# Optimization experiments

Measured on AMD Instinct MI355X. Metric: run time of the kernel, lower is better.

## Reference

```python
import jax, jax.numpy as jnp
import numpy as np

# ---- quantization constants (8-bit, per-tensor affine; representative values) ----
Q_MAX = 255.0
S_IN, Z_IN = 0.05, 128.0      # block input
S1, Z1 = 0.04, 128.0          # after expand 1x1 + hardswish
S2, Z2 = 0.04, 128.0          # after depthwise 5x5 + hardswish
S_SE1, Z_SE1 = 0.03, 128.0    # SE fc1 output
S_SE2, Z_SE2 = 1.0 / 255.0, 0.0  # SE fc2 hardsigmoid output in [0,1]
S_MUL, Z_MUL = 0.04, 128.0    # SE gated activation
S3, Z3 = 0.05, 128.0          # after project 1x1
S_OUT, Z_OUT = 0.06, 128.0    # after residual add
W_SCALE = 0.01                # symmetric per-tensor weight scale (zero_point = 0)
EXP_C = 576                   # expanded channels (depthwise groups)


def conv(x, w, stride=1, padding=0, groups=1):
    return jax.lax.conv_general_dilated(
        x, w, (stride, stride), [(padding, padding), (padding, padding)],
        feature_group_count=groups, dimension_numbers=('NCHW', 'OIHW', 'NCHW'))


def hardswish(x):
    return x * jnp.clip(x + 3.0, 0.0, 6.0) * (1.0 / 6.0)


def hardsigmoid(x):
    return jnp.clip(x + 3.0, 0.0, 6.0) * (1.0 / 6.0)


def qconv(x_q, w_q, b_q, s_in, z_in, s_out, z_out, stride=1, padding=0, groups=1, act=None):
    """Quantized conv: int-domain accumulation (simulated in fp32), fused activation
    on the dequantized accumulator, then requantize to [0, Q_MAX]."""
    acc = conv(x_q - z_in, w_q, stride, padding, groups) + b_q[None, :, None, None]
    deq = acc * (s_in * W_SCALE)  # dequantize accumulator
    if act == 'hardswish':
        deq = hardswish(deq)
    elif act == 'hardsigmoid':
        deq = hardsigmoid(deq)
    return jnp.clip(deq * (1.0 / s_out) + z_out, 0.0, Q_MAX)


def setup_inputs() -> dict:
    key = jax.random.key(0)
    ks = jax.random.split(key, 11)
    def qw(k, shape):  # int8-style symmetric weights stored as fp32 integers
        return jnp.round(jnp.clip(jax.random.normal(k, shape) * 40.0, -127.0, 127.0))
    def qb(k, n):      # int32-style bias in accumulator domain
        return jnp.round(jax.random.normal(k, (n,)) * 500.0)
    return {
        'x':      jnp.round(jax.random.uniform(ks[0], (64, 96, 28, 28)) * Q_MAX),
        'w_exp':  qw(ks[1], (576, 96, 1, 1)),  'b_exp':  qb(ks[2], 576),
        'w_dw':   qw(ks[3], (576, 1, 5, 5)),   'b_dw':   qb(ks[4], 576),
        'w_se1':  qw(ks[5], (144, 576, 1, 1)), 'b_se1':  qb(ks[6], 144),
        'w_se2':  qw(ks[7], (576, 144, 1, 1)), 'b_se2':  qb(ks[8], 576),
        'w_proj': qw(ks[9], (96, 576, 1, 1)),  'b_proj': qb(ks[10], 96),
    }


def reference(x, w_exp, b_exp, w_dw, b_dw, w_se1, b_se1, w_se2, b_se2, w_proj, b_proj):
    # expand 1x1 (+ hardswish)
    e = qconv(x, w_exp, b_exp, S_IN, Z_IN, S1, Z1, act='hardswish')
    # depthwise 5x5, padding=(5-1)//2=2, groups=expanded (+ hardswish)
    d = qconv(e, w_dw, b_dw, S1, Z1, S2, Z2, padding=2, groups=EXP_C, act='hardswish')
    # squeeze-excitation: global avg pool -> fc1 -> fc2(hardsigmoid) -> quantized mul
    pooled = jnp.mean(d, axis=(2, 3), keepdims=True)  # [N, 576, 1, 1]
    g1 = qconv(pooled, w_se1, b_se1, S2, Z2, S_SE1, Z_SE1)
    g2 = qconv(g1, w_se2, b_se2, S_SE1, Z_SE1, S_SE2, Z_SE2, act='hardsigmoid')
    gated = jnp.clip((g2 - Z_SE2) * (d - Z2) * (S_SE2 * S2 / S_MUL) + Z_MUL, 0.0, Q_MAX)
    # project 1x1 (linear)
    p = qconv(gated, w_proj, b_proj, S_MUL, Z_MUL, S3, Z3)
    # quantized residual add (stride=1, in==out channels -> use_res_connect)
    out = jnp.clip((x - Z_IN) * (S_IN / S_OUT) + (p - Z3) * (S3 / S_OUT) + Z_OUT, 0.0, Q_MAX)
    return out
```

## Files before the change

kernel.cpp:

```cpp
#include <hip/hip_runtime.h>

typedef _Float16 v8h __attribute__((ext_vector_type(8)));
typedef _Float16 v4h __attribute__((ext_vector_type(4)));
typedef _Float16 v2h __attribute__((ext_vector_type(2)));
typedef float v4f __attribute__((ext_vector_type(4)));

#define NB 64
#define CI 96
#define CE 576
#define CO 96
#define HW 784
#define SEC 144

#if defined(__has_builtin)
#if __has_builtin(__builtin_amdgcn_fdot2)
#define HAVE_FDOT2 1
#endif
#endif

__device__ __forceinline__ float fdot2(v2h a, v2h b, float c) {
#ifdef HAVE_FDOT2
  return __builtin_amdgcn_fdot2(a, b, c, false);
#else
  return (float)a[0] * (float)b[0] + ((float)a[1] * (float)b[1] + c);
#endif
}

__global__ __launch_bounds__(256) void k0x_pack(const float* __restrict__ x,
                                                const float* __restrict__ w_exp,
                                                const float* __restrict__ w_proj,
                                                _Float16* __restrict__ x_f,
                                                _Float16* __restrict__ x_h,
                                                _Float16* __restrict__ w_exp_h,
                                                _Float16* __restrict__ w_proj_h) {
  __shared__ _Float16 xl[112][40];
  const int tid = threadIdx.x;
  const int s = blockIdx.y;
  const int n = blockIdx.z;
  const int hw0 = blockIdx.x * 112;

  if (n == 0 && s == 0) {
    for (int i = blockIdx.x * 256 + tid; i < CE * CI; i += 7 * 256) {
      w_exp_h[i]  = (_Float16)w_exp[i];
      w_proj_h[i] = (_Float16)w_proj[i];
    }
  }

  for (int idx = tid; idx < 32 * 28; idx += 256) {
    int c_l = idx / 28, seg = idx % 28;
    int c = s * 32 + c_l;
    const float4 v = *(const float4*)&x[(n * CI + c) * HW + hw0 + seg * 4];
    v4h xh;
    xh[0] = (_Float16)(v.x - 128.0f);
    xh[1] = (_Float16)(v.y - 128.0f);
    xh[2] = (_Float16)(v.z - 128.0f);
    xh[3] = (_Float16)(v.w - 128.0f);
    int row = seg * 4;
    xl[row + 0][c_l] = xh[0];
    xl[row + 1][c_l] = xh[1];
    xl[row + 2][c_l] = xh[2];
    xl[row + 3][c_l] = xh[3];
    *(v4h*)&x_h[(n * CI + c) * HW + hw0 + seg * 4] = xh;
  }
  __syncthreads();

  for (int idx = tid; idx < 448; idx += 256) {
    int t_l = idx / 64, ln = idx % 64;
    int hw_l = t_l * 16 + (ln & 15), ci = (ln >> 4) * 8;
    v8h o = *(const v8h*)&xl[hw_l][ci];
    size_t t = (size_t)(blockIdx.x * 7 + t_l);
    *(v8h*)&x_f[(((size_t)n * 49 + t) * 3 + s) * 512 + ln * 8] = o;
  }
}

__global__ __launch_bounds__(448, 7) void k12_fused(const _Float16* __restrict__ x_f,
                                                    const _Float16* __restrict__ w_exp_h,
                                                    const float* __restrict__ b_exp,
                                                    const float* __restrict__ w_dw,
                                                    const float* __restrict__ b_dw,
                                                    _Float16* __restrict__ d_t,
                                                    float* __restrict__ d_sums2) {
  __shared__ _Float16 e_lds[16][18][42];
  __shared__ _Float16 d_tile[16][392];
  __shared__ _Float16 w_pairs[16][5][8];
  __shared__ float red[448];
  const int tid = threadIdx.x;
  const int n = blockIdx.z;
  const int h = blockIdx.y;
  const int c0 = blockIdx.x * 16;

  {
    unsigned long long* z = (unsigned long long*)&e_lds[0][0][0];
    for (int idx = tid; idx < 16 * 18 * 42 * 2 / 8; idx += 448) z[idx] = 0ull;
  }
  for (int idx = tid; idx < 640; idx += 448) {
    int c = idx / 40, r = idx % 40, dy = r / 8, k = r % 8;
    int tap = (k < 4) ? k : (k - 3);
    w_pairs[c][dy][k] = (_Float16)w_dw[(c0 + c) * 25 + dy * 5 + tap];
  }
  __syncthreads();

  const int wv = tid >> 6, lane = tid & 63;
  const int l15 = lane & 15, q = lane >> 4;

  {
    const _Float16* wrow = &w_exp_h[(c0 + l15) * CI + q * 8];
    v8h b0 = *(const v8h*)(wrow);
    v8h b1 = *(const v8h*)(wrow + 32);
    v8h b2 = *(const v8h*)(wrow + 64);
    const float bia = b_exp[c0 + l15];

    const int ir0 = 14 * h - 2;
    const _Float16* xb = x_f + (size_t)n * (49 * 3 * 512) + lane * 8;
#pragma unroll
    for (int i = 0; i < 4; ++i) {
      int t_l = wv + 7 * i;
      int t = 21 * h + t_l;
      const _Float16* xt = xb + (size_t)t * (3 * 512);
      v8h a0 = *(const v8h*)(xt);
      v8h a1 = *(const v8h*)(xt + 512);
      v8h a2 = *(const v8h*)(xt + 1024);
      v4f acc = (v4f){0.f, 0.f, 0.f, 0.f};
      acc = __builtin_amdgcn_mfma_f32_16x16x32_f16(a0, b0, acc, 0, 0, 0);
      acc = __builtin_amdgcn_mfma_f32_16x16x32_f16(a1, b1, acc, 0, 0, 0);
      acc = __builtin_amdgcn_mfma_f32_16x16x32_f16(a2, b2, acc, 0, 0, 0);
      int p = t * 16 + q * 4;
      int y = p / 28, xx = p - y * 28;
      int r_l = y - ir0;
      v4h ev;
#pragma unroll
      for (int r = 0; r < 4; ++r) {
        float deq = (acc[r] + bia) * 5.0e-4f;
        float cl  = fminf(fmaxf(deq + 3.0f, 0.0f), 6.0f);
        float evf = fminf(fmaxf(deq * cl * (25.0f / 6.0f), -128.0f), 127.0f);
        ev[r] = (_Float16)evf;
      }
      *(v4h*)&e_lds[l15][r_l][8 + xx] = ev;
    }
  }
  __syncthreads();

  const int c = tid / 28, l = tid % 28;
  v2h W01[5], W23[5], W12[5], W34[5];
  float W0s[5], W4s[5];
#pragma unroll
  for (int dy = 0; dy < 5; ++dy) {
    W01[dy] = *(const v2h*)&w_pairs[c][dy][0];
    W23[dy] = *(const v2h*)&w_pairs[c][dy][2];
    W12[dy] = *(const v2h*)&w_pairs[c][dy][4];
    W34[dy] = *(const v2h*)&w_pairs[c][dy][6];
    W0s[dy] = (float)W01[dy][0];
    W4s[dy] = (float)W34[dy][1];
  }
  const float bc = b_dw[c0 + c];

  float csum = 0.0f;
  {
    const int ry = l >> 1;
    const int bx = (l & 1) * 14;
    v2h P0[5], P1[5], P2[5], P3[5];
#pragma unroll
    for (int dy = 0; dy < 5; ++dy) {
      const _Float16* row = &e_lds[c][ry + dy][bx];
      P0[dy] = *(const v2h*)(row + 6);
      P1[dy] = *(const v2h*)(row + 8);
      P2[dy] = *(const v2h*)(row + 10);
      P3[dy] = *(const v2h*)(row + 12);
    }
#pragma unroll
    for (int xi = 0; xi < 3; ++xi) {
      const int x0 = bx + xi * 4;
      float o0 = bc, o1 = bc, o2 = bc, o3 = bc;
#pragma unroll
      for (int dy = 0; dy < 5; ++dy) {
        o0 = fdot2(P0[dy], W01[dy], o0);
        o0 = fdot2(P1[dy], W23[dy], o0);
        o0 += (float)P2[dy][0] * W4s[dy];
        o1 += (float)P0[dy][1] * W0s[dy];
        o1 = fdot2(P1[dy], W12[dy], o1);
        o1 = fdot2(P2[dy], W34[dy], o1);
        o2 = fdot2(P1[dy], W01[dy], o2);
        o2 = fdot2(P2[dy], W23[dy], o2);
        o2 += (float)P3[dy][0] * W4s[dy];
        o3 += (float)P1[dy][1] * W0s[dy];
        o3 = fdot2(P2[dy], W12[dy], o3);
        o3 = fdot2(P3[dy], W34[dy], o3);
      }
      float oo[4] = {o0, o1, o2, o3};
      v2h dva, dvb;
#pragma unroll
      for (int i = 0; i < 4; ++i) {
        float deq = oo[i] * 4.0e-4f;
        float cl  = fminf(fmaxf(deq + 3.0f, 0.0f), 6.0f);
        float dvv = fminf(fmaxf(deq * cl * (25.0f / 6.0f), -128.0f), 127.0f);
        if (i < 2) dva[i] = (_Float16)dvv; else dvb[i - 2] = (_Float16)dvv;
        csum += dvv;
      }
      *(v2h*)&d_tile[c][ry * 28 + x0]     = dva;
      *(v2h*)&d_tile[c][ry * 28 + x0 + 2] = dvb;
#pragma unroll
      for (int dy = 0; dy < 5; ++dy) {
        const _Float16* row = &e_lds[c][ry + dy][bx];
        P0[dy] = P2[dy];
        P1[dy] = P3[dy];
        P2[dy] = *(const v2h*)(row + x0 - bx + 14);
        P3[dy] = *(const v2h*)(row + x0 - bx + 16);
      }
    }
    {
      float o0 = bc, o1 = bc;
#pragma unroll
      for (int dy = 0; dy < 5; ++dy) {
        o0 = fdot2(P0[dy], W01[dy], o0);
        o0 = fdot2(P1[dy], W23[dy], o0);
        o0 += (float)P2[dy][0] * W4s[dy];
        o1 += (float)P0[dy][1] * W0s[dy];
        o1 = fdot2(P1[dy], W12[dy], o1);
        o1 = fdot2(P2[dy], W34[dy], o1);
      }
      v2h dv;
      float oo[2] = {o0, o1};
#pragma unroll
      for (int i = 0; i < 2; ++i) {
        float deq = oo[i] * 4.0e-4f;
        float cl  = fminf(fmaxf(deq + 3.0f, 0.0f), 6.0f);
        float dvv = fminf(fmaxf(deq * cl * (25.0f / 6.0f), -128.0f), 127.0f);
        dv[i] = (_Float16)dvv;
        csum += dvv;
      }
      *(v2h*)&d_tile[c][ry * 28 + bx + 12] = dv;
    }
  }
  red[tid] = csum;
  __syncthreads();

  if (tid < 392) {
    int hw_l = tid;
    const size_t obase = ((size_t)n * 72 + (c0 >> 3)) * 784 + 392 * h;
    v8h o0, o1;
#pragma unroll
    for (int j = 0; j < 8; ++j) { o0[j] = d_tile[j][hw_l]; o1[j] = d_tile[8 + j][hw_l]; }
    *(v8h*)&d_t[(obase + hw_l) * 8] = o0;
    *(v8h*)&d_t[(obase + 784 + hw_l) * 8] = o1;
  } else if (tid < 408) {
    int cc = tid - 392;
    float s = 0.f;
#pragma unroll
    for (int k = 0; k < 28; ++k) s += red[cc * 28 + k];
    d_sums2[((size_t)h * NB + n) * CE + c0 + cc] = s;
  }
}

__global__ __launch_bounds__(256) void k3a_fc1(const float* __restrict__ d_sums2,
                                               const float* __restrict__ w_se1,
                                               const float* __restrict__ b_se1,
                                               float* __restrict__ g1) {
  const int tid = threadIdx.x;
  const int wv = tid >> 6, lane = tid & 63;
  const int n = blockIdx.y;
  const int o = blockIdx.x * 4 + wv;
  const float* wrow = &w_se1[o * CE];
  const float* s0 = &d_sums2[(size_t)n * CE];
  const float* s1 = &d_sums2[((size_t)NB + n) * CE];
  float p = 0.f;
#pragma unroll
  for (int s = 0; s < 9; ++s) {
    int cc = lane + s * 64;
    p += wrow[cc] * (s0[cc] + s1[cc]);
  }
#pragma unroll
  for (int m = 32; m >= 1; m >>= 1) p += __shfl_xor(p, m);
  if (lane == 0) {
    float deq = (p * (1.0f / 784.0f) + b_se1[o]) * 4.0e-4f;
    g1[n * SEC + o] = fminf(fmaxf(deq * 33.3333333f + 128.0f, 0.0f), 255.0f) - 128.0f;
  }
}

__global__ __launch_bounds__(256) void k3b_fc2(const float* __restrict__ g1,
                                               const float* __restrict__ w_se2,
                                               const float* __restrict__ b_se2,
                                               _Float16* __restrict__ g2h) {
  const int tid = threadIdx.x;
  const int wv = tid >> 6, lane = tid & 63;
  const int n = blockIdx.y;
  const int o = blockIdx.x * 4 + wv;
  const float* wrow = &w_se2[o * SEC];
  const float* grow = &g1[n * SEC];
  float p = wrow[lane] * grow[lane] + wrow[lane + 64] * grow[lane + 64];
  if (lane < 16) p += wrow[lane + 128] * grow[lane + 128];
#pragma unroll
  for (int m = 32; m >= 1; m >>= 1) p += __shfl_xor(p, m);
  if (lane == 0) {
    float deq = (p + b_se2[o]) * 3.0e-4f;
    g2h[n * CE + o] =
        (_Float16)(fminf(fmaxf(deq + 3.0f, 0.0f), 6.0f) * (1.0f / 6.0f));
  }
}

__global__ __launch_bounds__(192) void k4_proj(const _Float16* __restrict__ d_t,
                                               const _Float16* __restrict__ g2h,
                                               const _Float16* __restrict__ w_proj_h,
                                               const float* __restrict__ b_proj,
                                               const _Float16* __restrict__ x_h,
                                               float* __restrict__ out) {
  const int tid = threadIdx.x;
  const int n = blockIdx.z;
  const int co0 = blockIdx.y * 48;
  const int hw0 = blockIdx.x * 112;
  const int wv = tid >> 6, lane = tid & 63;
  const int l15 = lane & 15, q = lane >> 4;

  v4f acc[7];
#pragma unroll
  for (int t = 0; t < 7; ++t) acc[t] = (v4f){0.f, 0.f, 0.f, 0.f};

  const _Float16* dbase = d_t + (((size_t)n * 72 + q) * 784 + hw0 + l15) * 8;
  const _Float16* abase = &w_proj_h[(co0 + wv * 16 + l15) * CE + q * 8];
  const _Float16* gbase = &g2h[(size_t)n * CE + q * 8];

  for (int ks = 0; ks < 18; ++ks) {
    v8h a = *(const v8h*)(abase + ks * 32);
    v8h g = *(const v8h*)(gbase + ks * 32);
    v8h ag = a * g;
    const _Float16* dk = dbase + (size_t)ks * (4 * 784 * 8);
#pragma unroll
    for (int t = 0; t < 7; ++t) {
      v8h b = *(const v8h*)(dk + t * (16 * 8));
      acc[t] = __builtin_amdgcn_mfma_f32_16x16x32_f16(ag, b, acc[t], 0, 0, 0);
    }
  }

  float bia[4];
#pragma unroll
  for (int r = 0; r < 4; ++r) bia[r] = b_proj[co0 + wv * 16 + q * 4 + r];

#pragma unroll
  for (int t = 0; t < 7; ++t) {
#pragma unroll
    for (int r = 0; r < 4; ++r) {
      int co = co0 + wv * 16 + q * 4 + r;
      int hw = hw0 + t * 16 + l15;
      float p = fminf(fmaxf((acc[t][r] + bia[r]) * 4.0e-4f * 20.0f + 128.0f, 0.0f), 255.0f);
      float xv = (float)x_h[(n * CO + co) * HW + hw];
      float o = xv * 0.8333333333f + (p - 128.0f) * 0.8333333333f + 128.0f;
      out[(n * CO + co) * HW + hw] = fminf(fmaxf(o, 0.0f), 255.0f);
    }
  }
}

extern "C" void kernel_launch(void* const* d_in, const int* in_sizes, int n_in,
                              void* d_out, int out_size, void* d_ws, size_t ws_size,
                              hipStream_t stream) {
  const float* x      = (const float*)d_in[0];
  const float* w_exp  = (const float*)d_in[1];
  const float* b_exp  = (const float*)d_in[2];
  const float* w_dw   = (const float*)d_in[3];
  const float* b_dw   = (const float*)d_in[4];
  const float* w_se1  = (const float*)d_in[5];
  const float* b_se1  = (const float*)d_in[6];
  const float* w_se2  = (const float*)d_in[7];
  const float* b_se2  = (const float*)d_in[8];
  const float* w_proj = (const float*)d_in[9];
  const float* b_proj = (const float*)d_in[10];
  float* out = (float*)d_out;

  char* ws = (char*)d_ws;
  const size_t SZ_W  = (size_t)CE * CI * 2;
  const size_t SZ_XF = (size_t)NB * 49 * 3 * 512 * 2;
  const size_t SZ_XH = (size_t)NB * CI * HW * 2;
  const size_t SZ_D  = (size_t)NB * CE * HW * 2;
  const size_t SZ_S2 = (size_t)2 * NB * CE * 4;
  const size_t SZ_S  = (size_t)NB * CE * 4;
  _Float16* w_exp_h  = (_Float16*)(ws);
  _Float16* w_proj_h = (_Float16*)(ws + SZ_W);
  _Float16* x_f      = (_Float16*)(ws + 2 * SZ_W);
  _Float16* x_h      = (_Float16*)(ws + 2 * SZ_W + SZ_XF);
  _Float16* d_t      = (_Float16*)(ws + 2 * SZ_W + SZ_XF + SZ_XH);
  float*    d_sums2  = (float*)   (ws + 2 * SZ_W + SZ_XF + SZ_XH + SZ_D);
  float*    g1       = (float*)   (ws + 2 * SZ_W + SZ_XF + SZ_XH + SZ_D + SZ_S2);
  _Float16* g2h      = (_Float16*)(ws + 2 * SZ_W + SZ_XF + SZ_XH + SZ_D + SZ_S2 + SZ_S);

  k0x_pack<<<dim3(7, 3, NB), 256, 0, stream>>>(x, w_exp, w_proj, x_f, x_h, w_exp_h, w_proj_h);
  k12_fused<<<dim3(36, 2, NB), 448, 0, stream>>>(x_f, w_exp_h, b_exp, w_dw, b_dw, d_t, d_sums2);
  k3a_fc1<<<dim3(36, NB), 256, 0, stream>>>(d_sums2, w_se1, b_se1, g1);
  k3b_fc2<<<dim3(144, NB), 256, 0, stream>>>(g1, w_se2, b_se2, g2h);
  k4_proj<<<dim3(7, 2, NB), 192, 0, stream>>>(d_t, g2h, w_proj_h, b_proj, x_h, out);
}
```

Before: 178.8 us.

## Use wave-aligned depthwise mapping with shuffle reduction and prefetch in projection

The fused expand+depthwise kernel moves from 448 to 512 threads so that each channel maps onto 32 lanes, with 4 idle lanes per channel. This allows the per-channel sum to be reduced with xor shuffles instead of an LDS array followed by a serial 28-element loop, removing the red buffer. The projection kernel software-pipelines its K loop by loading the next step's weights, gate values and activation tiles before issuing the current MFMAs, which hides global load latency at the cost of extra registers. The wider block wastes some lanes during the depthwise stage and could lower occupancy.

```diff
diff --git a/kernel.cpp b/kernel.cpp
--- a/kernel.cpp
+++ b/kernel.cpp
@@ -73,7 +73,7 @@
   }
 }
 
-__global__ __launch_bounds__(448, 7) void k12_fused(const _Float16* __restrict__ x_f,
+__global__ __launch_bounds__(512, 8) void k12_fused(const _Float16* __restrict__ x_f,
                                                     const _Float16* __restrict__ w_exp_h,
                                                     const float* __restrict__ b_exp,
                                                     const float* __restrict__ w_dw,
@@ -83,7 +83,6 @@
   __shared__ _Float16 e_lds[16][18][42];
   __shared__ _Float16 d_tile[16][392];
   __shared__ _Float16 w_pairs[16][5][8];
-  __shared__ float red[448];
   const int tid = threadIdx.x;
   const int n = blockIdx.z;
   const int h = blockIdx.y;
@@ -91,9 +90,9 @@
 
   {
     unsigned long long* z = (unsigned long long*)&e_lds[0][0][0];
-    for (int idx = tid; idx < 16 * 18 * 42 * 2 / 8; idx += 448) z[idx] = 0ull;
-  }
-  for (int idx = tid; idx < 640; idx += 448) {
+    for (int idx = tid; idx < 16 * 18 * 42 * 2 / 8; idx += 512) z[idx] = 0ull;
+  }
+  for (int idx = tid; idx < 640; idx += 512) {
     int c = idx / 40, r = idx % 40, dy = r / 8, k = r % 8;
     int tap = (k < 4) ? k : (k - 3);
     w_pairs[c][dy][k] = (_Float16)w_dw[(c0 + c) * 25 + dy * 5 + tap];
@@ -112,9 +111,7 @@
 
     const int ir0 = 14 * h - 2;
     const _Float16* xb = x_f + (size_t)n * (49 * 3 * 512) + lane * 8;
-#pragma unroll
-    for (int i = 0; i < 4; ++i) {
-      int t_l = wv + 7 * i;
+    for (int t_l = wv; t_l < 28; t_l += 8) {
       int t = 21 * h + t_l;
       const _Float16* xt = xb + (size_t)t * (3 * 512);
       v8h a0 = *(const v8h*)(xt);
@@ -140,7 +137,7 @@
   }
   __syncthreads();
 
-  const int c = tid / 28, l = tid % 28;
+  const int c = tid >> 5, l = tid & 31;
   v2h W01[5], W23[5], W12[5], W34[5];
   float W0s[5], W4s[5];
 #pragma unroll
@@ -155,7 +152,7 @@
   const float bc = b_dw[c0 + c];
 
   float csum = 0.0f;
-  {
+  if (l < 28) {
     const int ry = l >> 1;
     const int bx = (l & 1) * 14;
     v2h P0[5], P1[5], P2[5], P3[5];
@@ -231,23 +228,19 @@
       *(v2h*)&d_tile[c][ry * 28 + bx + 12] = dv;
     }
   }
-  red[tid] = csum;
+#pragma unroll
+  for (int m = 16; m >= 1; m >>= 1) csum += __shfl_xor(csum, m);
+  if (l == 0) d_sums2[((size_t)h * NB + n) * CE + c0 + c] = csum;
+
   __syncthreads();
-
+  const size_t obase = ((size_t)n * 72 + (c0 >> 3)) * 784 + 392 * h;
   if (tid < 392) {
     int hw_l = tid;
-    const size_t obase = ((size_t)n * 72 + (c0 >> 3)) * 784 + 392 * h;
     v8h o0, o1;
 #pragma unroll
     for (int j = 0; j < 8; ++j) { o0[j] = d_tile[j][hw_l]; o1[j] = d_tile[8 + j][hw_l]; }
     *(v8h*)&d_t[(obase + hw_l) * 8] = o0;
     *(v8h*)&d_t[(obase + 784 + hw_l) * 8] = o1;
-  } else if (tid < 408) {
-    int cc = tid - 392;
-    float s = 0.f;
-#pragma unroll
-    for (int k = 0; k < 28; ++k) s += red[cc * 28 + k];
-    d_sums2[((size_t)h * NB + n) * CE + c0 + cc] = s;
   }
 }
 
@@ -317,17 +310,36 @@
   const _Float16* dbase = d_t + (((size_t)n * 72 + q) * 784 + hw0 + l15) * 8;
   const _Float16* abase = &w_proj_h[(co0 + wv * 16 + l15) * CE + q * 8];
   const _Float16* gbase = &g2h[(size_t)n * CE + q * 8];
-
-  for (int ks = 0; ks < 18; ++ks) {
-    v8h a = *(const v8h*)(abase + ks * 32);
-    v8h g = *(const v8h*)(gbase + ks * 32);
+  const size_t KS = (size_t)4 * 784 * 8;
+
+  v8h a = *(const v8h*)(abase);
+  v8h g = *(const v8h*)(gbase);
+  v8h b[7];
+#pragma unroll
+  for (int t = 0; t < 7; ++t) b[t] = *(const v8h*)(dbase + t * 128);
+
+  for (int ks = 0; ks < 17; ++ks) {
+    v8h a2 = *(const v8h*)(abase + (ks + 1) * 32);
+    v8h g2 = *(const v8h*)(gbase + (ks + 1) * 32);
+    v8h b2[7];
+    const _Float16* dk2 = dbase + (size_t)(ks + 1) * KS;
+#pragma unroll
+    for (int t = 0; t < 7; ++t) b2[t] = *(const v8h*)(dk2 + t * 128);
+
     v8h ag = a * g;
-    const _Float16* dk = dbase + (size_t)ks * (4 * 784 * 8);
-#pragma unroll
-    for (int t = 0; t < 7; ++t) {
-      v8h b = *(const v8h*)(dk + t * (16 * 8));
-      acc[t] = __builtin_amdgcn_mfma_f32_16x16x32_f16(ag, b, acc[t], 0, 0, 0);
-    }
+#pragma unroll
+    for (int t = 0; t < 7; ++t)
+      acc[t] = __builtin_amdgcn_mfma_f32_16x16x32_f16(ag, b[t], acc[t], 0, 0, 0);
+
+    a = a2; g = g2;
+#pragma unroll
+    for (int t = 0; t < 7; ++t) b[t] = b2[t];
+  }
+  {
+    v8h ag = a * g;
+#pragma unroll
+    for (int t = 0; t < 7; ++t)
+      acc[t] = __builtin_amdgcn_mfma_f32_16x16x32_f16(ag, b[t], acc[t], 0, 0, 0);
   }
 
   float bia[4];
@@ -381,7 +393,7 @@
   _Float16* g2h      = (_Float16*)(ws + 2 * SZ_W + SZ_XF + SZ_XH + SZ_D + SZ_S2 + SZ_S);
 
   k0x_pack<<<dim3(7, 3, NB), 256, 0, stream>>>(x, w_exp, w_proj, x_f, x_h, w_exp_h, w_proj_h);
-  k12_fused<<<dim3(36, 2, NB), 448, 0, stream>>>(x_f, w_exp_h, b_exp, w_dw, b_dw, d_t, d_sums2);
+  k12_fused<<<dim3(36, 2, NB), 512, 0, stream>>>(x_f, w_exp_h, b_exp, w_dw, b_dw, d_t, d_sums2);
   k3a_fc1<<<dim3(36, NB), 256, 0, stream>>>(d_sums2, w_se1, b_se1, g1);
   k3b_fc2<<<dim3(144, NB), 256, 0, stream>>>(g1, w_se2, b_se2, g2h);
   k4_proj<<<dim3(7, 2, NB), 192, 0, stream>>>(d_t, g2h, w_proj_h, b_proj, x_h, out);
```

Measured after the change: 175.7 us. No clear change (-1.8%).
